# Performance work log

Measured on AMD Instinct MI355X. Metric: run time of the kernel, lower is better.

Reference implementation:

```python
import jax, jax.numpy as jnp
import numpy as np

EMBED_DIM = 1536
NUM_HEADS = 12
HEAD_DIM = EMBED_DIM // NUM_HEADS  # 128
SEQ = 2048
EPS = 1e-5


def rms_norm(x, w):
    # x: (..., HEAD_DIM)
    var = jnp.mean(jnp.square(x), axis=-1, keepdims=True)
    return x * jax.lax.rsqrt(var + EPS) * w


def apply_rotary(x, cos, sin):
    # x: (b, s, h, d); cos/sin: (s, d/2) -> broadcast (1, s, 1, d/2)
    d2 = cos.shape[-1]
    c = cos[None, :, None, :]
    s_ = sin[None, :, None, :]
    x1, x2 = x[..., :d2], x[..., d2:]
    return jnp.concatenate([x1 * c - x2 * s_, x2 * c + x1 * s_], axis=-1)


def setup_inputs() -> dict:
    key = jax.random.key(0)
    ks = jax.random.split(key, 10)
    x = jax.random.normal(ks[0], (SEQ, 1, EMBED_DIM), dtype=jnp.float32)
    cu_seqlens = jnp.array([0, SEQ // 2, SEQ], dtype=jnp.int32)
    # rotary tables for positions 0..SEQ-1, rotary dim = HEAD_DIM
    inv_freq = 1.0 / (10000.0 ** (jnp.arange(0, HEAD_DIM, 2, dtype=jnp.float32) / HEAD_DIM))
    pos = jnp.arange(SEQ, dtype=jnp.float32)
    freqs = pos[:, None] * inv_freq[None, :]  # (s, d/2)
    rotary_pos_emb_cos = jnp.cos(freqs)
    rotary_pos_emb_sin = jnp.sin(freqs)
    scale = 0.02
    w_qkv = jax.random.normal(ks[1], (EMBED_DIM, 3 * EMBED_DIM), dtype=jnp.float32) * scale
    b_qkv = jnp.zeros((3 * EMBED_DIM,), dtype=jnp.float32)
    q_norm_w = jnp.ones((HEAD_DIM,), dtype=jnp.float32)
    k_norm_w = jnp.ones((HEAD_DIM,), dtype=jnp.float32)
    w_proj = jax.random.normal(ks[2], (EMBED_DIM, EMBED_DIM), dtype=jnp.float32) * scale
    b_proj = jnp.zeros((EMBED_DIM,), dtype=jnp.float32)
    return {
        'x': x, 'cu_seqlens': cu_seqlens,
        'rotary_pos_emb_cos': rotary_pos_emb_cos, 'rotary_pos_emb_sin': rotary_pos_emb_sin,
        'w_qkv': w_qkv, 'b_qkv': b_qkv, 'q_norm_w': q_norm_w, 'k_norm_w': k_norm_w,
        'w_proj': w_proj, 'b_proj': b_proj,
    }


def reference(x, cu_seqlens, rotary_pos_emb_cos, rotary_pos_emb_sin,
              w_qkv, b_qkv, q_norm_w, k_norm_w, w_proj, b_proj):
    s, b, e = x.shape
    h, d = NUM_HEADS, HEAD_DIM
    qkv = jnp.einsum('sbe,ef->sbf', x, w_qkv) + b_qkv  # (s, b, 3e)
    q, k, v = jnp.split(qkv, 3, axis=2)
    q = q.reshape(s, b, h, d)
    k = k.reshape(s, b, h, d)
    v = v.reshape(s, b, h, d)
    # per-head RMSNorm on q/k
    q = rms_norm(q, q_norm_w)
    k = rms_norm(k, k_norm_w)
    # (s, b, h, d) -> (b, s, h, d)
    q = jnp.transpose(q, (1, 0, 2, 3))
    k = jnp.transpose(k, (1, 0, 2, 3))
    v = jnp.transpose(v, (1, 0, 2, 3))
    q = apply_rotary(q, rotary_pos_emb_cos, rotary_pos_emb_sin)
    k = apply_rotary(k, rotary_pos_emb_cos, rotary_pos_emb_sin)
    # varlen (block-diagonal, non-causal) attention via segment mask
    pos = jnp.arange(s)
    seg = jnp.searchsorted(cu_seqlens[1:], pos, side='right')  # (s,)
    mask = seg[:, None] == seg[None, :]  # (s, s)
    scale = d ** -0.5
    scores = jnp.einsum('bqhd,bkhd->bhqk', q, k) * scale  # (b, h, s, s)
    scores = jnp.where(mask[None, None, :, :], scores, jnp.finfo(scores.dtype).min)
    attn = jax.nn.softmax(scores, axis=-1)
    ctx = jnp.einsum('bhqk,bkhd->bqhd', attn, v)  # (b, s, h, d)
    # (b, s, h, d) -> (s, b, h*d)
    ctx = jnp.transpose(ctx, (1, 0, 2, 3)).reshape(s, b, h * d)
    out = jnp.einsum('sbe,ef->sbf', ctx, w_proj) + b_proj
    return out
```

## Files before the change

### kernel.cpp

```cpp
#include <hip/hip_runtime.h>
#include <hip/hip_bf16.h>
#include <stdint.h>

#define S_LEN 2048
#define EMB   1536
#define NH    12
#define HD    128
#define N3    4608
#define RMS_EPS 1e-5f
#define ATTN_SCALE 0.08838834764831845f
#define SPLIT 2

typedef short short8_t __attribute__((ext_vector_type(8)));
typedef float f32x4    __attribute__((ext_vector_type(4)));

typedef __attribute__((address_space(1))) const void g1_void;
typedef __attribute__((address_space(3))) void l3_void;

__device__ __forceinline__ void gload_lds16(const void* g, void* l) {
  __builtin_amdgcn_global_load_lds((g1_void*)g, (l3_void*)l, 16, 0, 0);
}

__device__ __forceinline__ short f2bf(float f) {
  union { float f; unsigned u; } v; v.f = f;
  unsigned r = (v.u + 0x7FFFu + ((v.u >> 16) & 1u)) >> 16;
  return (short)(r & 0xFFFFu);
}
__device__ __forceinline__ float bf2f(short s) {
  union { unsigned u; float f; } v; v.u = ((unsigned)(unsigned short)s) << 16;
  return v.f;
}

__global__ __launch_bounds__(256) void k_cvt_bf16(const float* __restrict__ in,
                                                  short* __restrict__ out, int n) {
  int i = (blockIdx.x * 256 + threadIdx.x) * 4;
  if (i + 3 < n) {
    float4 v = *(const float4*)(in + i);
    short4 o;
    o.x = f2bf(v.x); o.y = f2bf(v.y); o.z = f2bf(v.z); o.w = f2bf(v.w);
    *(short4*)(out + i) = o;
  }
}

__global__ __launch_bounds__(256) void k_transpose_cvt(const float* __restrict__ W,
                                                       short* __restrict__ Wt,
                                                       int K, int N) {
  __shared__ float t[32][33];
  int n0 = blockIdx.x * 32, k0 = blockIdx.y * 32;
  int tx = threadIdx.x, ty = threadIdx.y;
#pragma unroll
  for (int r = 0; r < 4; ++r) {
    int k = ty + r * 8;
    t[k][tx] = W[(size_t)(k0 + k) * N + n0 + tx];
  }
  __syncthreads();
#pragma unroll
  for (int r = 0; r < 4; ++r) {
    int j = ty + r * 8;
    Wt[(size_t)(n0 + j) * K + k0 + tx] = f2bf(t[tx][j]);
  }
}

template<bool OBF>
__global__ __launch_bounds__(256) void k_gemm_v2(const short* __restrict__ A,
                                                 const short* __restrict__ Bt,
                                                 const float* __restrict__ bias,
                                                 void* __restrict__ Cv,
                                                 int M, int N, int K) {
  __shared__ short lds[2][2][128 * 64];
  const int tid = threadIdx.x;
  const int lane = tid & 63, wid = tid >> 6;
  const int wr = (wid >> 1) * 64, wc = (wid & 1) * 64;
  const int bn = blockIdx.x * 128, bm = blockIdx.y * 128;
  const int lr = lane & 15, lg = lane >> 4;
  const int swz = (lr & 7) << 4;

  const int srow = lane >> 3;
  const int skc  = ((lane & 7) ^ srow) * 8;

  f32x4 acc[4][4] = {};
  const int nk = K >> 6;

#pragma unroll
  for (int it = 0; it < 4; ++it) {
    int seg = wid * 4 + it;
    int row = seg * 8 + srow;
    gload_lds16(A  + (size_t)(bm + row) * K + skc, &lds[0][0][seg * 512]);
    gload_lds16(Bt + (size_t)(bn + row) * K + skc, &lds[0][1][seg * 512]);
  }
  __syncthreads();

  int cur = 0;
  for (int t = 0; t < nk; ++t) {
    if (t + 1 < nk) {
      const int kt = (t + 1) << 6;
#pragma unroll
      for (int it = 0; it < 4; ++it) {
        int seg = wid * 4 + it;
        int row = seg * 8 + srow;
        gload_lds16(A  + (size_t)(bm + row) * K + kt + skc, &lds[cur ^ 1][0][seg * 512]);
        gload_lds16(Bt + (size_t)(bn + row) * K + kt + skc, &lds[cur ^ 1][1][seg * 512]);
      }
    }
    const char* baseA = (const char*)&lds[cur][0][0];
    const char* baseB = (const char*)&lds[cur][1][0];
#pragma unroll
    for (int kk = 0; kk < 2; ++kk) {
      short8_t af[4], bfr[4];
#pragma unroll
      for (int m = 0; m < 4; ++m) {
        int row = wr + m * 16 + lr;
        af[m] = *(const short8_t*)(baseA + ((row * 128 + kk * 64 + lg * 16) ^ swz));
      }
#pragma unroll
      for (int n = 0; n < 4; ++n) {
        int row = wc + n * 16 + lr;
        bfr[n] = *(const short8_t*)(baseB + ((row * 128 + kk * 64 + lg * 16) ^ swz));
      }
#pragma unroll
      for (int m = 0; m < 4; ++m)
#pragma unroll
        for (int n = 0; n < 4; ++n)
          acc[m][n] = __builtin_amdgcn_mfma_f32_16x16x32_bf16(af[m], bfr[n], acc[m][n], 0, 0, 0);
    }
    __syncthreads();
    cur ^= 1;
  }

#pragma unroll
  for (int m = 0; m < 4; ++m)
#pragma unroll
    for (int n = 0; n < 4; ++n) {
      int col = bn + wc + n * 16 + lr;
      float bv = bias[col];
#pragma unroll
      for (int r = 0; r < 4; ++r) {
        int row = bm + wr + m * 16 + lg * 4 + r;
        float v = acc[m][n][r] + bv;
        if (OBF) ((short*)Cv)[(size_t)row * N + col] = f2bf(v);
        else     ((float*)Cv)[(size_t)row * N + col] = v;
      }
    }
}

__global__ __launch_bounds__(256) void k_post(const short* __restrict__ qkv,
                                              const float* __restrict__ cosv,
                                              const float* __restrict__ sinv,
                                              const float* __restrict__ qw,
                                              const float* __restrict__ kw,
                                              short* __restrict__ qb,
                                              short* __restrict__ kb,
                                              short* __restrict__ vt) {
  __shared__ short ldsv[64 * 130];
  const int h = blockIdx.x, s0 = blockIdx.y * 64;
  const int t = threadIdx.x;
  const int r = t >> 2, j = t & 3;
  const int s = s0 + r;
  const size_t rowbase = (size_t)s * N3 + h * HD;

  {
    const short* vp = qkv + rowbase + 2 * EMB + j * 32;
#pragma unroll
    for (int i4 = 0; i4 < 4; ++i4)
      *(short8_t*)&ldsv[r * 130 + j * 32 + i4 * 8] = *(const short8_t*)(vp + i4 * 8);
  }

#pragma unroll
  for (int qk = 0; qk < 2; ++qk) {
    const short* p = qkv + rowbase + qk * EMB + j * 32;
    const float* w = qk ? kw : qw;
    float v[32];
#pragma unroll
    for (int i4 = 0; i4 < 4; ++i4) {
      short8_t x = *(const short8_t*)(p + i4 * 8);
#pragma unroll
      for (int e = 0; e < 8; ++e) v[i4 * 8 + e] = bf2f(x[e]);
    }
    float ss = 0.f;
#pragma unroll
    for (int i = 0; i < 32; ++i) ss += v[i] * v[i];
    ss += __shfl_xor(ss, 1);
    ss += __shfl_xor(ss, 2);
    float rsq = rsqrtf(ss * (1.0f / HD) + RMS_EPS);
#pragma unroll
    for (int i = 0; i < 32; ++i) v[i] = v[i] * rsq * w[j * 32 + i];
    const float* cp = cosv + (size_t)s * 64 + (j & 1) * 32;
    const float* sp = sinv + (size_t)s * 64 + (j & 1) * 32;
    short out[32];
#pragma unroll
    for (int i = 0; i < 32; ++i) {
      float part = __shfl_xor(v[i], 2);
      float c = cp[i], sn = sp[i];
      float o = (j < 2) ? (v[i] * c - part * sn) : (v[i] * c + part * sn);
      out[i] = f2bf(o);
    }
    short* dst = (qk ? kb : qb) + ((size_t)h * S_LEN + s) * HD + j * 32;
#pragma unroll
    for (int i4 = 0; i4 < 4; ++i4) {
      short8_t o8;
#pragma unroll
      for (int e = 0; e < 8; ++e) o8[e] = out[i4 * 8 + e];
      *(short8_t*)(dst + i4 * 8) = o8;
    }
  }

  __syncthreads();
  const int sl = t & 63, wv = t >> 6;
#pragma unroll
  for (int it = 0; it < 32; ++it) {
    int d = it * 4 + wv;
    vt[((size_t)h * HD + d) * S_LEN + s0 + sl] = ldsv[sl * 130 + d];
  }
}

__global__ __launch_bounds__(512, 2) void k_attn(const short* __restrict__ qb,
                                                 const short* __restrict__ kb,
                                                 const short* __restrict__ vt,
                                                 const int* __restrict__ cu, int nseg,
                                                 short* __restrict__ Opart,
                                                 float* __restrict__ mlpart) {
  __shared__ short ldsK[2][64 * 128];
  __shared__ short ldsV[2][128 * 64];
  __shared__ short ldsP[8 * 16 * 64];

  const int wg = blockIdx.x;
  const int member = wg / 48;
  const int c = wg % 48;
  const int p = c & 1;
  const int h = c >> 2;
  const int qt = ((c >> 1) & 1) * 8 + member;

  const int q0 = qt * 128;
  const int tid = threadIdx.x, l = tid & 63, w = tid >> 6;
  const int lr = l & 15, lg = l >> 4;

  const short* kb_h = kb + (size_t)h * S_LEN * HD;
  const short* vt_h = vt + (size_t)h * HD * S_LEN;

  int rs[4], re[4];
  float m[4], lsum[4];
#pragma unroll
  for (int r = 0; r < 4; ++r) {
    int row = q0 + w * 16 + lg * 4 + r;
    int seg = 0;
    for (int i = 1; i <= nseg; ++i) if (row >= cu[i]) seg = i;
    rs[r] = (seg == 0) ? 0 : cu[seg];
    re[r] = (seg < nseg) ? cu[seg + 1] : S_LEN;
    m[r] = -INFINITY;
    lsum[r] = 0.f;
  }

  int seg0 = 0, seg1 = 0;
  for (int i = 1; i <= nseg; ++i) {
    if (q0 >= cu[i]) seg0 = i;
    if (q0 + 127 >= cu[i]) seg1 = i;
  }
  const int ks = (seg0 == 0) ? 0 : cu[seg0];
  const int ke = (seg1 < nseg) ? cu[seg1 + 1] : S_LEN;
  const int kt0 = (ks >> 6) << 6;
  const int nt = (ke - kt0 + 63) >> 6;
  const int tpb = (nt + SPLIT - 1) / SPLIT;
  const int tb0 = p * tpb;
  const int tb1 = (tb0 + tpb < nt) ? tb0 + tpb : nt;

  const int kseg_row = l >> 4;
  const int vseg_row = l >> 3;
  const int sck = ((l & 15) ^ ((l >> 4) & 3)) * 8;
  const int scv_base = l & 7;

  short8_t qf[4];
  {
    int srow = q0 + w * 16 + lr;
    const short* qp = qb + ((size_t)h * S_LEN + srow) * HD;
#pragma unroll
    for (int kk = 0; kk < 4; ++kk)
      qf[kk] = *(const short8_t*)(qp + kk * 32 + lg * 8);
  }

  f32x4 cacc[8] = {};

#define STAGE(kt_, buf_)                                                          \
  {                                                                               \
    const int kt__ = (kt_);                                                       \
    _Pragma("unroll")                                                             \
    for (int it = 0; it < 2; ++it) {                                              \
      int s = w * 2 + it;                                                         \
      int lrow = s * 4 + kseg_row;                                                \
      int sk = ((l & 15) ^ (lrow & 7)) * 8;                                       \
      gload_lds16(kb_h + (size_t)(kt__ + lrow) * HD + sk, &ldsK[buf_][s * 512]);  \
      int drow = s * 8 + vseg_row;                                                \
      int sv = ((l & 7) ^ (drow & 7)) * 8;                                        \
      gload_lds16(vt_h + (size_t)drow * S_LEN + kt__ + sv, &ldsV[buf_][s * 512]); \
    }                                                                             \
  }

  if (tb0 < tb1)     STAGE(kt0 + tb0 * 64, 0);
  if (tb0 + 1 < tb1) {
    STAGE(kt0 + (tb0 + 1) * 64, 1);
    asm volatile("s_waitcnt vmcnt(4)" ::: "memory");
  } else {
    asm volatile("s_waitcnt vmcnt(0)" ::: "memory");
  }
  __builtin_amdgcn_s_barrier();

  int cur = 0;
  for (int ti = tb0; ti < tb1; ++ti) {
    const int kt = kt0 + ti * 64;
    const char* bK = (const char*)&ldsK[cur][0];
    const char* bV = (const char*)&ldsV[cur][0];

    f32x4 sacc[4] = {};
    __builtin_amdgcn_s_setprio(1);
#pragma unroll
    for (int n = 0; n < 4; ++n) {
#pragma unroll
      for (int kk = 0; kk < 4; ++kk) {
        int row = n * 16 + lr;
        int byte = row * 256 + (kk * 32 + lg * 8) * 2;
        byte ^= (row & 7) << 4;
        short8_t kf = *(const short8_t*)(bK + byte);
        sacc[n] = __builtin_amdgcn_mfma_f32_16x16x32_bf16(qf[kk], kf, sacc[n], 0, 0, 0);
      }
    }
    __builtin_amdgcn_s_setprio(0);

#pragma unroll
    for (int n = 0; n < 4; ++n) {
      int key = kt + n * 16 + lr;
#pragma unroll
      for (int r = 0; r < 4; ++r) {
        float x = sacc[n][r] * ATTN_SCALE;
        sacc[n][r] = (key >= rs[r] && key < re[r]) ? x : -1e30f;
      }
    }
    float alpha[4];
#pragma unroll
    for (int r = 0; r < 4; ++r) {
      float tm = fmaxf(fmaxf(sacc[0][r], sacc[1][r]), fmaxf(sacc[2][r], sacc[3][r]));
#pragma unroll
      for (int off = 1; off < 16; off <<= 1) tm = fmaxf(tm, __shfl_xor(tm, off));
      float mn = fmaxf(m[r], tm);
      alpha[r] = __expf(m[r] - mn);
      m[r] = mn;
      float ls = 0.f;
#pragma unroll
      for (int n = 0; n < 4; ++n) {
        float pv = __expf(sacc[n][r] - mn);
        sacc[n][r] = pv;
        ls += pv;
      }
#pragma unroll
      for (int off = 1; off < 16; off <<= 1) ls += __shfl_xor(ls, off);
      lsum[r] = lsum[r] * alpha[r] + ls;
    }
#pragma unroll
    for (int n = 0; n < 8; ++n)
#pragma unroll
      for (int r = 0; r < 4; ++r) cacc[n][r] *= alpha[r];

#pragma unroll
    for (int n = 0; n < 4; ++n)
#pragma unroll
      for (int r = 0; r < 4; ++r) {
        int prow = lg * 4 + r;
        int pcol = n * 16 + lr;
        int byte = prow * 128 + pcol * 2;
        byte ^= (prow & 7) << 4;
        *(short*)((char*)ldsP + w * 2048 + byte) = f2bf(sacc[n][r]);
      }

    __builtin_amdgcn_s_setprio(1);
#pragma unroll
    for (int kk = 0; kk < 2; ++kk) {
      int byteP = lr * 128 + (kk * 32 + lg * 8) * 2;
      byteP ^= (lr & 7) << 4;
      short8_t pf = *(const short8_t*)((const char*)ldsP + w * 2048 + byteP);
#pragma unroll
      for (int n = 0; n < 8; ++n) {
        int d = n * 16 + lr;
        int byteV = d * 128 + (kk * 32 + lg * 8) * 2;
        byteV ^= (d & 7) << 4;
        short8_t vf = *(const short8_t*)(bV + byteV);
        cacc[n] = __builtin_amdgcn_mfma_f32_16x16x32_bf16(pf, vf, cacc[n], 0, 0, 0);
      }
    }
    __builtin_amdgcn_s_setprio(0);

    __builtin_amdgcn_s_barrier();
    if (ti + 2 < tb1) {
      STAGE(kt0 + (ti + 2) * 64, cur);
      asm volatile("s_waitcnt vmcnt(4)" ::: "memory");
    } else {
      asm volatile("s_waitcnt vmcnt(0)" ::: "memory");
    }
    __builtin_amdgcn_s_barrier();
    cur ^= 1;
  }
#undef STAGE

  const int b = (h * 16 + qt) * SPLIT + p;
#pragma unroll
  for (int r = 0; r < 4; ++r) {
    int qrow = w * 16 + lg * 4 + r;
#pragma unroll
    for (int n = 0; n < 8; ++n)
      Opart[(size_t)b * 16384 + qrow * 128 + n * 16 + lr] = f2bf(cacc[n][r]);
  }
  if (lr == 0) {
#pragma unroll
    for (int r = 0; r < 4; ++r) {
      int qrow = w * 16 + lg * 4 + r;
      mlpart[(size_t)b * 256 + qrow] = m[r];
      mlpart[(size_t)b * 256 + 128 + qrow] = lsum[r];
    }
  }
}

__global__ __launch_bounds__(512) void k_combine(const short* __restrict__ Opart,
                                                 const float* __restrict__ ml,
                                                 short* __restrict__ ctx) {
  const int h = blockIdx.x, qt = blockIdx.y, t = threadIdx.x;
  const int r = t >> 2, j = t & 3;
  const int b0 = (h * 16 + qt) * SPLIT;

  float mp[SPLIT], lp[SPLIT], wp[SPLIT];
  float M = -INFINITY;
#pragma unroll
  for (int p = 0; p < SPLIT; ++p) {
    mp[p] = ml[(size_t)(b0 + p) * 256 + r];
    lp[p] = ml[(size_t)(b0 + p) * 256 + 128 + r];
    M = fmaxf(M, mp[p]);
  }
  float L = 0.f;
#pragma unroll
  for (int p = 0; p < SPLIT; ++p) {
    wp[p] = __expf(mp[p] - M);
    L += lp[p] * wp[p];
  }
  const float inv = 1.0f / L;

  float acc[32];
#pragma unroll
  for (int i = 0; i < 32; ++i) acc[i] = 0.f;
#pragma unroll
  for (int p = 0; p < SPLIT; ++p) {
    const short* src = Opart + (size_t)(b0 + p) * 16384 + r * 128 + j * 32;
#pragma unroll
    for (int i4 = 0; i4 < 4; ++i4) {
      short8_t v = *(const short8_t*)(src + i4 * 8);
#pragma unroll
      for (int e = 0; e < 8; ++e) acc[i4 * 8 + e] += wp[p] * bf2f(v[e]);
    }
  }

  short* dst = ctx + (size_t)(qt * 128 + r) * EMB + h * HD + j * 32;
#pragma unroll
  for (int i4 = 0; i4 < 4; ++i4) {
    short8_t o8;
#pragma unroll
    for (int e = 0; e < 8; ++e) o8[e] = f2bf(acc[i4 * 8 + e] * inv);
    *(short8_t*)(dst + i4 * 8) = o8;
  }
}

extern "C" void kernel_launch(void* const* d_in, const int* in_sizes, int n_in,
                              void* d_out, int out_size, void* d_ws, size_t ws_size,
                              hipStream_t stream) {
  const float* x      = (const float*)d_in[0];
  const int*   cu     = (const int*)d_in[1];
  const float* cosv   = (const float*)d_in[2];
  const float* sinv   = (const float*)d_in[3];
  const float* w_qkv  = (const float*)d_in[4];
  const float* b_qkv  = (const float*)d_in[5];
  const float* q_norm = (const float*)d_in[6];
  const float* k_norm = (const float*)d_in[7];
  const float* w_proj = (const float*)d_in[8];
  const float* b_proj = (const float*)d_in[9];
  const int nseg = in_sizes[1] - 1;

  char* ws = (char*)d_ws;
  short* xb     = (short*)(ws);
  short* wqkvT  = (short*)(ws + 6291456);
  short* wprojT = (short*)(ws + 20447232);
  short* qkv16  = (short*)(ws + 25165824);
  short* qb     = (short*)(ws + 44040192);
  short* kb     = (short*)(ws + 50331648);
  short* vt     = (short*)(ws + 56623104);
  short* ctxb   = (short*)(ws + 62914560);
  short* Opart  = qkv16;
  float* mlpart = (float*)ws;

  k_cvt_bf16<<<(S_LEN * EMB) / 1024, 256, 0, stream>>>(x, xb, S_LEN * EMB);
  k_transpose_cvt<<<dim3(N3 / 32, EMB / 32), dim3(32, 8), 0, stream>>>(w_qkv, wqkvT, EMB, N3);
  k_transpose_cvt<<<dim3(EMB / 32, EMB / 32), dim3(32, 8), 0, stream>>>(w_proj, wprojT, EMB, EMB);
  k_gemm_v2<true><<<dim3(N3 / 128, S_LEN / 128), 256, 0, stream>>>(xb, wqkvT, b_qkv, qkv16, S_LEN, N3, EMB);
  k_post<<<dim3(NH, S_LEN / 64), 256, 0, stream>>>(qkv16, cosv, sinv, q_norm, k_norm, qb, kb, vt);
  k_attn<<<dim3(NH * (S_LEN / 128) * SPLIT), 512, 0, stream>>>(qb, kb, vt, cu, nseg, Opart, mlpart);
  k_combine<<<dim3(NH, S_LEN / 128), 512, 0, stream>>>(Opart, mlpart, ctxb);
  k_gemm_v2<false><<<dim3(EMB / 128, S_LEN / 128), 256, 0, stream>>>(ctxb, wprojT, b_proj, (float*)d_out, S_LEN, EMB, EMB);
}
```

Baseline: 156.5 us.

## Transpose QK^T MFMA, use exp2 softmax with lazy rescaling and fast-path masking

```diff
diff --git a/kernel.cpp b/kernel.cpp
--- a/kernel.cpp
+++ b/kernel.cpp
@@ -10,6 +10,8 @@
 #define RMS_EPS 1e-5f
 #define ATTN_SCALE 0.08838834764831845f
 #define SPLIT 2
+#define LOG2E 1.44269504088896f
+#define DEFER_THR 11.5416f
 
 typedef short short8_t __attribute__((ext_vector_type(8)));
 typedef float f32x4    __attribute__((ext_vector_type(4)));
@@ -237,18 +239,12 @@
   const short* kb_h = kb + (size_t)h * S_LEN * HD;
   const short* vt_h = vt + (size_t)h * HD * S_LEN;
 
-  int rs[4], re[4];
-  float m[4], lsum[4];
-#pragma unroll
-  for (int r = 0; r < 4; ++r) {
-    int row = q0 + w * 16 + lg * 4 + r;
-    int seg = 0;
-    for (int i = 1; i <= nseg; ++i) if (row >= cu[i]) seg = i;
-    rs[r] = (seg == 0) ? 0 : cu[seg];
-    re[r] = (seg < nseg) ? cu[seg + 1] : S_LEN;
-    m[r] = -INFINITY;
-    lsum[r] = 0.f;
-  }
+  const int qrow_sm = q0 + w * 16 + lr;
+  int segq = 0;
+  for (int i = 1; i <= nseg; ++i) if (qrow_sm >= cu[i]) segq = i;
+  const int rs_s = (segq == 0) ? 0 : cu[segq];
+  const int re_s = (segq < nseg) ? cu[segq + 1] : S_LEN;
+  float m = -INFINITY, lsum = 0.f;
 
   int seg0 = 0, seg1 = 0;
   for (int i = 1; i <= nseg; ++i) {
@@ -265,8 +261,6 @@
 
   const int kseg_row = l >> 4;
   const int vseg_row = l >> 3;
-  const int sck = ((l & 15) ^ ((l >> 4) & 3)) * 8;
-  const int scv_base = l & 7;
 
   short8_t qf[4];
   {
@@ -278,6 +272,7 @@
   }
 
   f32x4 cacc[8] = {};
+  const float SC2 = ATTN_SCALE * LOG2E;
 
 #define STAGE(kt_, buf_)                                                          \
   {                                                                               \
@@ -319,55 +314,68 @@
         int byte = row * 256 + (kk * 32 + lg * 8) * 2;
         byte ^= (row & 7) << 4;
         short8_t kf = *(const short8_t*)(bK + byte);
-        sacc[n] = __builtin_amdgcn_mfma_f32_16x16x32_bf16(qf[kk], kf, sacc[n], 0, 0, 0);
+        sacc[n] = __builtin_amdgcn_mfma_f32_16x16x32_bf16(kf, qf[kk], sacc[n], 0, 0, 0);
       }
     }
     __builtin_amdgcn_s_setprio(0);
 
+    if (__all((kt >= rs_s) && (kt + 64 <= re_s))) {
+#pragma unroll
+      for (int n = 0; n < 4; ++n)
+#pragma unroll
+        for (int r = 0; r < 4; ++r) sacc[n][r] *= SC2;
+    } else {
+#pragma unroll
+      for (int n = 0; n < 4; ++n) {
+        int kbase = kt + n * 16 + lg * 4;
+#pragma unroll
+        for (int r = 0; r < 4; ++r) {
+          int key = kbase + r;
+          float x = sacc[n][r] * SC2;
+          sacc[n][r] = (key >= rs_s && key < re_s) ? x : -1e30f;
+        }
+      }
+    }
+
+    float tm = sacc[0][0];
+#pragma unroll
+    for (int n = 0; n < 4; ++n)
+#pragma unroll
+      for (int r = 0; r < 4; ++r) tm = fmaxf(tm, sacc[n][r]);
+    tm = fmaxf(tm, __shfl_xor(tm, 16));
+    tm = fmaxf(tm, __shfl_xor(tm, 32));
+
+    if (!__all(tm <= m + DEFER_THR)) {
+      float mn = fmaxf(m, tm);
+      float alpha = exp2f(m - mn);
+      m = mn;
+      lsum *= alpha;
+      float a[4];
+#pragma unroll
+      for (int r = 0; r < 4; ++r) a[r] = __shfl(alpha, lg * 4 + r);
+#pragma unroll
+      for (int n = 0; n < 8; ++n)
+#pragma unroll
+        for (int r = 0; r < 4; ++r) cacc[n][r] *= a[r];
+    }
+
+    float ls = 0.f;
 #pragma unroll
     for (int n = 0; n < 4; ++n) {
-      int key = kt + n * 16 + lr;
-#pragma unroll
-      for (int r = 0; r < 4; ++r) {
-        float x = sacc[n][r] * ATTN_SCALE;
-        sacc[n][r] = (key >= rs[r] && key < re[r]) ? x : -1e30f;
-      }
-    }
-    float alpha[4];
-#pragma unroll
-    for (int r = 0; r < 4; ++r) {
-      float tm = fmaxf(fmaxf(sacc[0][r], sacc[1][r]), fmaxf(sacc[2][r], sacc[3][r]));
-#pragma unroll
-      for (int off = 1; off < 16; off <<= 1) tm = fmaxf(tm, __shfl_xor(tm, off));
-      float mn = fmaxf(m[r], tm);
-      alpha[r] = __expf(m[r] - mn);
-      m[r] = mn;
-      float ls = 0.f;
-#pragma unroll
-      for (int n = 0; n < 4; ++n) {
-        float pv = __expf(sacc[n][r] - mn);
-        sacc[n][r] = pv;
-        ls += pv;
-      }
-#pragma unroll
-      for (int off = 1; off < 16; off <<= 1) ls += __shfl_xor(ls, off);
-      lsum[r] = lsum[r] * alpha[r] + ls;
-    }
-#pragma unroll
-    for (int n = 0; n < 8; ++n)
-#pragma unroll
-      for (int r = 0; r < 4; ++r) cacc[n][r] *= alpha[r];
-
-#pragma unroll
-    for (int n = 0; n < 4; ++n)
-#pragma unroll
-      for (int r = 0; r < 4; ++r) {
-        int prow = lg * 4 + r;
-        int pcol = n * 16 + lr;
-        int byte = prow * 128 + pcol * 2;
-        byte ^= (prow & 7) << 4;
-        *(short*)((char*)ldsP + w * 2048 + byte) = f2bf(sacc[n][r]);
-      }
+      short4 p4;
+      float p0 = exp2f(sacc[n][0] - m);
+      float p1 = exp2f(sacc[n][1] - m);
+      float p2 = exp2f(sacc[n][2] - m);
+      float p3 = exp2f(sacc[n][3] - m);
+      ls += (p0 + p1) + (p2 + p3);
+      p4.x = f2bf(p0); p4.y = f2bf(p1); p4.z = f2bf(p2); p4.w = f2bf(p3);
+      int byte = lr * 128 + (n * 16 + lg * 4) * 2;
+      byte ^= (lr & 7) << 4;
+      *(short4*)((char*)ldsP + w * 2048 + byte) = p4;
+    }
+    ls += __shfl_xor(ls, 16);
+    ls += __shfl_xor(ls, 32);
+    lsum += ls;
 
     __builtin_amdgcn_s_setprio(1);
 #pragma unroll
@@ -406,13 +414,9 @@
     for (int n = 0; n < 8; ++n)
       Opart[(size_t)b * 16384 + qrow * 128 + n * 16 + lr] = f2bf(cacc[n][r]);
   }
-  if (lr == 0) {
-#pragma unroll
-    for (int r = 0; r < 4; ++r) {
-      int qrow = w * 16 + lg * 4 + r;
-      mlpart[(size_t)b * 256 + qrow] = m[r];
-      mlpart[(size_t)b * 256 + 128 + qrow] = lsum[r];
-    }
+  if (lg == 0) {
+    mlpart[(size_t)b * 256 + w * 16 + lr] = m;
+    mlpart[(size_t)b * 256 + 128 + w * 16 + lr] = lsum;
   }
 }
 
@@ -434,7 +438,7 @@
   float L = 0.f;
 #pragma unroll
   for (int p = 0; p < SPLIT; ++p) {
-    wp[p] = __expf(mp[p] - M);
+    wp[p] = exp2f(mp[p] - M);
     L += lp[p] * wp[p];
   }
   const float inv = 1.0f / L;
```

Result: faster. 147.2 us (median of 2 runs) (-6.0%).
